# Kernel tuning notes

Measured on AMD Instinct MI355X. Metric: run time of the kernel, lower is better.

## Reference

```python
import jax, jax.numpy as jnp
import numpy as np

EMB = 768
HEADS = 12
HEAD_DIM = EMB // HEADS


def setup_inputs() -> dict:
    key = jax.random.key(0)
    k1, k2, k3, k4 = jax.random.split(key, 4)
    x = jax.random.normal(k1, (8, 1024, EMB), dtype=jnp.float32)
    # Dense kernels, TF default glorot-ish scale approximated with small normals
    w_qkv = jax.random.normal(k2, (EMB, 3 * EMB), dtype=jnp.float32) * 0.02
    w_out = jax.random.normal(k3, (EMB, EMB), dtype=jnp.float32) * 0.02
    b_out = jnp.zeros((EMB,), dtype=jnp.float32)
    return {"x": x, "w_qkv": w_qkv, "w_out": w_out, "b_out": b_out}


def reference(x, w_qkv, w_out, b_out):
    B, S, E = x.shape
    qkv = jnp.einsum("bse,ef->bsf", x, w_qkv)                 # [B,S,3E]
    qkv = qkv.reshape(B, S, 3, HEADS, HEAD_DIM)
    qkv = jnp.transpose(qkv, (2, 0, 3, 1, 4))                  # [3,B,H,S,D]
    q, k, v = qkv[0], qkv[1], qkv[2]
    scale = jnp.float32(HEAD_DIM) ** -0.5
    # Blocked loop in source computes exact full (non-causal) attention:
    # every query block attends to all keys -> equivalent to standard SDPA.
    scores = jnp.einsum("bhqd,bhkd->bhqk", q, k) * scale       # [B,H,S,S]
    probs = jax.nn.softmax(scores, axis=-1)
    out = jnp.einsum("bhqk,bhkd->bhqd", probs, v)              # [B,H,S,D]
    out = jnp.transpose(out, (0, 2, 1, 3)).reshape(B, S, E)
    return jnp.einsum("bse,ef->bsf", out, w_out) + b_out
```

## Files before the change

kernel.cpp:

```cpp
#include <hip/hip_runtime.h>

typedef float f32x4 __attribute__((ext_vector_type(4)));
typedef short bf16x8 __attribute__((ext_vector_type(8)));

#define MFMA_BF16(a, b, c) __builtin_amdgcn_mfma_f32_16x16x32_bf16((a), (b), (c), 0, 0, 0)

#define GLDS16(gp, lp) __builtin_amdgcn_global_load_lds( \
    (const __attribute__((address_space(1))) unsigned int*)(gp), \
    (__attribute__((address_space(3))) unsigned int*)(lp), 16, 0, 0)

__device__ __forceinline__ ushort f2bf(float f) {
    unsigned int u = __float_as_uint(f);
    return (ushort)((u + 0x7FFFu + ((u >> 16) & 1u)) >> 16);
}

__device__ __forceinline__ float fexp2(float x) {
#if __has_builtin(__builtin_amdgcn_exp2f)
    return __builtin_amdgcn_exp2f(x);
#else
    return exp2f(x);
#endif
}

__global__ __launch_bounds__(256) void prep_kernel(
    const float* __restrict__ x, const float* __restrict__ wq, const float* __restrict__ wo,
    ushort* __restrict__ xb, ushort* __restrict__ wqbt, ushort* __restrict__ wobt)
{
    __shared__ float tile[32][33];
    const int bid = blockIdx.x;
    if (bid < 2048) {
        const float4* src = (const float4*)x;
        ushort4* dst = (ushort4*)xb;
        for (int i = bid * 256 + threadIdx.x; i < 1572864; i += 2048 * 256) {
            float4 v = src[i];
            ushort4 o;
            o.x = f2bf(v.x); o.y = f2bf(v.y); o.z = f2bf(v.z); o.w = f2bf(v.w);
            dst[i] = o;
        }
        return;
    }
    const float* src; ushort* dst; int K, N, bx, by;
    if (bid < 3776) {
        const int L = bid - 2048;
        src = wq; dst = wqbt; K = 768; N = 2304; bx = L % 72; by = L / 72;
    } else {
        const int L = bid - 3776;
        src = wo; dst = wobt; K = 768; N = 768; bx = L % 24; by = L / 24;
    }
    const int n0 = bx * 32, k0 = by * 32;
    const int c = threadIdx.x & 31, rb = threadIdx.x >> 5;
    #pragma unroll
    for (int i = 0; i < 4; ++i)
        tile[i * 8 + rb][c] = src[(size_t)(k0 + i * 8 + rb) * N + n0 + c];
    __syncthreads();
    #pragma unroll
    for (int i = 0; i < 4; ++i) {
        int nr = i * 8 + rb;
        dst[(size_t)(n0 + nr) * K + k0 + c] = f2bf(tile[c][nr]);
    }
}

__global__ __launch_bounds__(512) void gemm_qkv_mfma(
    const ushort* __restrict__ A, const ushort* __restrict__ Bt,
    ushort* __restrict__ Qo, ushort* __restrict__ Ko, ushort* __restrict__ Vo)
{
    __shared__ ushort Al[3][16384];
    __shared__ ushort Bl[3][8192];
    const int tid = threadIdx.x, lane = tid & 63;
    const int wv = tid >> 6, lo = lane & 15, hi = lane >> 4;
    const int wr = wv >> 1, wc = wv & 1;
    const int L = blockIdx.x;
    const int nid = (L & 7) * 72 + (L >> 3);
    const int n0 = (nid % 18) * 128, m0 = (nid / 18) * 256;

    auto stageA = [&](int bi, int k0) {
        #pragma unroll
        for (int it = 0; it < 4; ++it) {
            const int p = it * 512 + tid;
            const int row = p >> 3, ch = (p & 7) ^ (row & 7);
            GLDS16(A + (size_t)(m0 + row) * 768 + k0 + ch * 8,
                   &Al[bi][(it * 512 + (tid & 448)) * 8]);
        }
    };
    auto stageB = [&](int bi, int k0) {
        #pragma unroll
        for (int it = 0; it < 2; ++it) {
            const int p = it * 512 + tid;
            const int row = p >> 3, ch = (p & 7) ^ (row & 7);
            GLDS16(Bt + (size_t)(n0 + row) * 768 + k0 + ch * 8,
                   &Bl[bi][(it * 512 + (tid & 448)) * 8]);
        }
    };

    f32x4 acc[4][4];
    #pragma unroll
    for (int i = 0; i < 4; ++i)
        #pragma unroll
        for (int j = 0; j < 4; ++j)
            acc[i][j] = (f32x4){0.f, 0.f, 0.f, 0.f};

    const int region = n0 / 768;
    const int h = ((n0 % 768) >> 6) + wc;

    stageA(0, 0);  stageB(0, 0);
    stageA(1, 64); stageB(1, 64);

    int cur = 0;
    for (int t = 0; t < 12; ++t) {
        if (t < 11) asm volatile("s_waitcnt vmcnt(6)" ::: "memory");
        else        asm volatile("s_waitcnt vmcnt(0)" ::: "memory");
        __builtin_amdgcn_s_barrier();
        asm volatile("" ::: "memory");
        if (t + 2 < 12) {
            const int nb = cur ? cur - 1 : 2;
            stageA(nb, (t + 2) * 64);
            stageB(nb, (t + 2) * 64);
        }
        #pragma unroll
        for (int ks = 0; ks < 2; ++ks) {
            bf16x8 af[4], bfr[4];
            #pragma unroll
            for (int i = 0; i < 4; ++i) {
                const int ra = wr * 64 + i * 16 + lo;
                af[i] = *(const bf16x8*)&Al[cur][ra * 64 + (((ks * 4 + hi) ^ (ra & 7)) * 8)];
                const int rb = wc * 64 + i * 16 + lo;
                bfr[i] = *(const bf16x8*)&Bl[cur][rb * 64 + (((ks * 4 + hi) ^ (rb & 7)) * 8)];
            }
            if (region == 2) {
                #pragma unroll
                for (int mi = 0; mi < 4; ++mi)
                    #pragma unroll
                    for (int nj = 0; nj < 4; ++nj)
                        acc[mi][nj] = MFMA_BF16(af[mi], bfr[nj], acc[mi][nj]);
            } else {
                #pragma unroll
                for (int mi = 0; mi < 4; ++mi)
                    #pragma unroll
                    for (int nj = 0; nj < 4; ++nj)
                        acc[mi][nj] = MFMA_BF16(bfr[nj], af[mi], acc[mi][nj]);
            }
        }
        cur = cur == 2 ? 0 : cur + 1;
    }

    if (region == 2) {
        #pragma unroll
        for (int mi = 0; mi < 4; ++mi) {
            const int m4 = m0 + wr * 64 + mi * 16 + hi * 4;
            const int b = m4 >> 10, s = m4 & 1023;
            #pragma unroll
            for (int nj = 0; nj < 4; ++nj) {
                const int d = nj * 16 + lo;
                ushort4 pk;
                pk.x = f2bf(acc[mi][nj][0]); pk.y = f2bf(acc[mi][nj][1]);
                pk.z = f2bf(acc[mi][nj][2]); pk.w = f2bf(acc[mi][nj][3]);
                *(ushort4*)&Vo[((size_t)(b * 12 + h) * 64 + d) * 1024 + s] = pk;
            }
        }
    } else {
        ushort* dst = region ? Ko : Qo;
        const float sc = region ? 1.0f : 0.18033688011112042f;
        #pragma unroll
        for (int mi = 0; mi < 4; ++mi) {
            const int s_idx = m0 + wr * 64 + mi * 16 + lo;
            const int b = s_idx >> 10, s = s_idx & 1023;
            const size_t base = ((size_t)(b * 12 + h) * 1024 + s) * 64;
            #pragma unroll
            for (int nj = 0; nj < 4; ++nj) {
                ushort4 pk;
                pk.x = f2bf(acc[mi][nj][0] * sc); pk.y = f2bf(acc[mi][nj][1] * sc);
                pk.z = f2bf(acc[mi][nj][2] * sc); pk.w = f2bf(acc[mi][nj][3] * sc);
                *(ushort4*)&dst[base + nj * 16 + hi * 4] = pk;
            }
        }
    }
}

__global__ __launch_bounds__(256) void attn_mfma_kernel(
    const ushort* __restrict__ Qg, const ushort* __restrict__ Kg,
    const ushort* __restrict__ Vg, ushort* __restrict__ AO)
{
    __shared__ ushort Kl[2][4096];
    __shared__ ushort Vl[2][4096];
    __shared__ ushort Pl[4][32 * 72];

    const int tid = threadIdx.x, lane = tid & 63;
    const int wv = tid >> 6, lo = lane & 15, hi = lane >> 4;
    const int L = blockIdx.x;
    const int xcd = L & 7, g = L >> 3;
    const int qb = g / 12;
    const int bh = xcd * 12 + (g % 12);
    const int b = bh / 12, h = bh % 12;
    const size_t kvbase = (size_t)bh * (1024 * 64);

    bf16x8 qa[2][2];
    const int qrow0 = qb * 128 + wv * 32;
    #pragma unroll
    for (int mi = 0; mi < 2; ++mi)
        #pragma unroll
        for (int ks = 0; ks < 2; ++ks)
            qa[mi][ks] = *(const bf16x8*)&Qg[kvbase + (size_t)(qrow0 + mi * 16 + lo) * 64 + ks * 32 + hi * 8];

    f32x4 o[2][4];
    float lp[2] = {0.f, 0.f};
    #pragma unroll
    for (int mi = 0; mi < 2; ++mi)
        #pragma unroll
        for (int dj = 0; dj < 4; ++dj) o[mi][dj] = (f32x4){0.f, 0.f, 0.f, 0.f};

    auto stage = [&](int bi, int kt) {
        #pragma unroll
        for (int it = 0; it < 2; ++it) {
            const int p = it * 256 + tid;
            const int row = p >> 3, ch = (p & 7) ^ (row & 7);
            GLDS16(Kg + kvbase + (size_t)(kt + row) * 64 + ch * 8, &Kl[bi][(it * 256 + (tid & 192)) * 8]);
        }
        #pragma unroll
        for (int it = 0; it < 2; ++it) {
            const int p = it * 256 + tid;
            const int row = p >> 3, ch = (p & 7) ^ (row & 7);
            GLDS16(Vg + kvbase + (size_t)row * 1024 + kt + ch * 8, &Vl[bi][(it * 256 + (tid & 192)) * 8]);
        }
    };

    stage(0, 0);
    __syncthreads();

    for (int t = 0; t < 16; ++t) {
        const int cur = t & 1;
        if (t < 15) stage(cur ^ 1, (t + 1) * 64);

        f32x4 s[2][4];
        #pragma unroll
        for (int mi = 0; mi < 2; ++mi)
            #pragma unroll
            for (int nj = 0; nj < 4; ++nj) s[mi][nj] = (f32x4){0.f, 0.f, 0.f, 0.f};
        #pragma unroll
        for (int ks = 0; ks < 2; ++ks) {
            bf16x8 kb[4];
            #pragma unroll
            for (int nj = 0; nj < 4; ++nj) {
                const int key = nj * 16 + lo, c = ks * 4 + hi;
                kb[nj] = *(const bf16x8*)&Kl[cur][key * 64 + ((c ^ (key & 7)) * 8)];
            }
            #pragma unroll
            for (int mi = 0; mi < 2; ++mi)
                #pragma unroll
                for (int nj = 0; nj < 4; ++nj)
                    s[mi][nj] = MFMA_BF16(kb[nj], qa[mi][ks], s[mi][nj]);
        }

        #pragma unroll
        for (int mi = 0; mi < 2; ++mi) {
            #pragma unroll
            for (int nj = 0; nj < 4; ++nj) {
                const unsigned int u0 = __float_as_uint(fexp2(s[mi][nj][0]));
                const unsigned int u1 = __float_as_uint(fexp2(s[mi][nj][1]));
                const unsigned int u2 = __float_as_uint(fexp2(s[mi][nj][2]));
                const unsigned int u3 = __float_as_uint(fexp2(s[mi][nj][3]));
                const float t0 = __uint_as_float(u0 & 0xFFFF0000u);
                const float t1 = __uint_as_float(u1 & 0xFFFF0000u);
                const float t2 = __uint_as_float(u2 & 0xFFFF0000u);
                const float t3 = __uint_as_float(u3 & 0xFFFF0000u);
                lp[mi] += (t0 + t1) + (t2 + t3);
                ushort4 pk;
                pk.x = (ushort)(u0 >> 16); pk.y = (ushort)(u1 >> 16);
                pk.z = (ushort)(u2 >> 16); pk.w = (ushort)(u3 >> 16);
                *(ushort4*)&Pl[wv][(mi * 16 + lo) * 72 + nj * 16 + hi * 4] = pk;
            }
        }

        #pragma unroll
        for (int ks = 0; ks < 2; ++ks) {
            bf16x8 pa[2];
            #pragma unroll
            for (int mi = 0; mi < 2; ++mi)
                pa[mi] = *(const bf16x8*)&Pl[wv][(mi * 16 + lo) * 72 + ks * 32 + hi * 8];
            bf16x8 vb[4];
            #pragma unroll
            for (int dj = 0; dj < 4; ++dj) {
                const int d = dj * 16 + lo, c = ks * 4 + hi;
                vb[dj] = *(const bf16x8*)&Vl[cur][d * 64 + ((c ^ (d & 7)) * 8)];
            }
            #pragma unroll
            for (int mi = 0; mi < 2; ++mi)
                #pragma unroll
                for (int dj = 0; dj < 4; ++dj)
                    o[mi][dj] = MFMA_BF16(pa[mi], vb[dj], o[mi][dj]);
        }
        __syncthreads();
    }

    #pragma unroll
    for (int mi = 0; mi < 2; ++mi) {
        float l = lp[mi];
        l += __shfl_xor(l, 16);
        l += __shfl_xor(l, 32);
        #pragma unroll
        for (int r = 0; r < 4; ++r) {
            const float lr = __shfl(l, hi * 4 + r, 16);
            const float rcp = 1.0f / lr;
            const int srow = qrow0 + mi * 16 + hi * 4 + r;
            #pragma unroll
            for (int dj = 0; dj < 4; ++dj)
                AO[((size_t)(b * 1024 + srow)) * 768 + h * 64 + dj * 16 + lo] =
                    f2bf(o[mi][dj][r] * rcp);
        }
    }
}

__global__ __launch_bounds__(256) void gemm_out_mfma(
    const ushort* __restrict__ A, const ushort* __restrict__ Bt,
    const float* __restrict__ bias, float* __restrict__ C)
{
    __shared__ ushort Al[2][4096];
    __shared__ ushort Bl[2][4096];
    const int tid = threadIdx.x, lane = tid & 63;
    const int wv = tid >> 6, lo = lane & 15, hi = lane >> 4;
    const int wr = wv >> 1, wc = wv & 1;
    const int L = blockIdx.x + 6 * blockIdx.y;
    const int nid = (L & 7) * 48 + (L >> 3);
    const int n0 = (nid % 6) * 128, m0 = (nid / 6) * 128;

    auto stage = [&](int bi, int k0) {
        #pragma unroll
        for (int it = 0; it < 2; ++it) {
            const int p = it * 256 + tid;
            const int row = p >> 2, ch = (p & 3) ^ ((row >> 1) & 3);
            GLDS16(A + (size_t)(m0 + row) * 768 + k0 + ch * 8, &Al[bi][(it * 256 + (tid & 192)) * 8]);
            GLDS16(Bt + (size_t)(n0 + row) * 768 + k0 + ch * 8, &Bl[bi][(it * 256 + (tid & 192)) * 8]);
        }
    };

    f32x4 acc[4][4];
    #pragma unroll
    for (int i = 0; i < 4; ++i)
        #pragma unroll
        for (int j = 0; j < 4; ++j)
            acc[i][j] = (f32x4){0.f, 0.f, 0.f, 0.f};

    stage(0, 0);
    __syncthreads();
    for (int kt = 0; kt < 24; ++kt) {
        const int cur = kt & 1;
        if (kt < 23) stage(cur ^ 1, (kt + 1) * 32);
        bf16x8 af[4], bfr[4];
        #pragma unroll
        for (int i = 0; i < 4; ++i) {
            const int ra = wr * 64 + i * 16 + lo;
            af[i] = *(const bf16x8*)&Al[cur][ra * 32 + ((hi ^ ((ra >> 1) & 3)) * 8)];
            const int rb = wc * 64 + i * 16 + lo;
            bfr[i] = *(const bf16x8*)&Bl[cur][rb * 32 + ((hi ^ ((rb >> 1) & 3)) * 8)];
        }
        #pragma unroll
        for (int mi = 0; mi < 4; ++mi)
            #pragma unroll
            for (int nj = 0; nj < 4; ++nj)
                acc[mi][nj] = MFMA_BF16(bfr[nj], af[mi], acc[mi][nj]);
        __syncthreads();
    }

    const int ncol0 = n0 + wc * 64;
    #pragma unroll
    for (int mi = 0; mi < 4; ++mi) {
        const int m = m0 + wr * 64 + mi * 16 + lo;
        #pragma unroll
        for (int nj = 0; nj < 4; ++nj) {
            const int nb = ncol0 + nj * 16 + hi * 4;
            const float4 bv = *reinterpret_cast<const float4*>(&bias[nb]);
            float4 ov;
            ov.x = acc[mi][nj][0] + bv.x; ov.y = acc[mi][nj][1] + bv.y;
            ov.z = acc[mi][nj][2] + bv.z; ov.w = acc[mi][nj][3] + bv.w;
            *reinterpret_cast<float4*>(&C[(size_t)m * 768 + nb]) = ov;
        }
    }
}

extern "C" void kernel_launch(void* const* d_in, const int* in_sizes, int n_in,
                              void* d_out, int out_size, void* d_ws, size_t ws_size,
                              hipStream_t stream) {
    const float* x     = (const float*)d_in[0];
    const float* w_qkv = (const float*)d_in[1];
    const float* w_out = (const float*)d_in[2];
    const float* b_out = (const float*)d_in[3];
    float* out = (float*)d_out;

    (void)in_sizes; (void)n_in; (void)out_size; (void)ws_size;

    ushort* xb   = (ushort*)d_ws;
    ushort* wqbt = xb + 6291456;
    ushort* wobt = wqbt + 1769472;
    ushort* Qs   = wobt + 589824;
    ushort* Ks   = Qs + 6291456;
    ushort* Vt   = Ks + 6291456;
    ushort* AO   = Vt + 6291456;

    prep_kernel<<<4352, 256, 0, stream>>>(x, w_qkv, w_out, xb, wqbt, wobt);
    gemm_qkv_mfma<<<576, 512, 0, stream>>>(xb, wqbt, Qs, Ks, Vt);
    attn_mfma_kernel<<<768, 256, 0, stream>>>(Qs, Ks, Vt, AO);
    gemm_out_mfma<<<dim3(6, 64), 256, 0, stream>>>(AO, wobt, b_out, out);
}
```

Before: 134.6 us.

## Retile QKV GEMM to 128x128 double-buffered blocks and unify out-projection pipeline

The QKV projection GEMM moves from 512-thread 256x128 tiles with a triple-buffered LDS ring to 256-thread 128x128 tiles with double buffering, doubling the grid to 1152 blocks. Each k-step now ends with an extra barrier before the next tile is staged. The output-projection GEMM adopts the same pipeline: K-step 64 instead of 32, an 8-chunk XOR swizzle, two tiles prefetched ahead, and a 1D grid. The aim is more blocks and waves per CU and fewer barrier iterations in the out GEMM, at the cost of less reuse of each tile and one extra barrier per step.

```diff
diff --git a/kernel.cpp b/kernel.cpp
--- a/kernel.cpp
+++ b/kernel.cpp
@@ -60,35 +60,33 @@
     }
 }
 
-__global__ __launch_bounds__(512) void gemm_qkv_mfma(
+__global__ __launch_bounds__(256) void gemm_qkv_mfma(
     const ushort* __restrict__ A, const ushort* __restrict__ Bt,
     ushort* __restrict__ Qo, ushort* __restrict__ Ko, ushort* __restrict__ Vo)
 {
-    __shared__ ushort Al[3][16384];
-    __shared__ ushort Bl[3][8192];
+    __shared__ ushort Al[2][8192];
+    __shared__ ushort Bl[2][8192];
     const int tid = threadIdx.x, lane = tid & 63;
     const int wv = tid >> 6, lo = lane & 15, hi = lane >> 4;
     const int wr = wv >> 1, wc = wv & 1;
     const int L = blockIdx.x;
-    const int nid = (L & 7) * 72 + (L >> 3);
-    const int n0 = (nid % 18) * 128, m0 = (nid / 18) * 256;
-
-    auto stageA = [&](int bi, int k0) {
+    const int nid = (L & 7) * 144 + (L >> 3);
+    const int n0 = (nid % 18) * 128, m0 = (nid / 18) * 128;
+
+    auto stage = [&](int bi, int k0) {
         #pragma unroll
         for (int it = 0; it < 4; ++it) {
-            const int p = it * 512 + tid;
+            const int p = it * 256 + tid;
             const int row = p >> 3, ch = (p & 7) ^ (row & 7);
             GLDS16(A + (size_t)(m0 + row) * 768 + k0 + ch * 8,
-                   &Al[bi][(it * 512 + (tid & 448)) * 8]);
-        }
-    };
-    auto stageB = [&](int bi, int k0) {
-        #pragma unroll
-        for (int it = 0; it < 2; ++it) {
-            const int p = it * 512 + tid;
+                   &Al[bi][(it * 256 + (tid & 192)) * 8]);
+        }
+        #pragma unroll
+        for (int it = 0; it < 4; ++it) {
+            const int p = it * 256 + tid;
             const int row = p >> 3, ch = (p & 7) ^ (row & 7);
             GLDS16(Bt + (size_t)(n0 + row) * 768 + k0 + ch * 8,
-                   &Bl[bi][(it * 512 + (tid & 448)) * 8]);
+                   &Bl[bi][(it * 256 + (tid & 192)) * 8]);
         }
     };
 
@@ -102,20 +100,16 @@
     const int region = n0 / 768;
     const int h = ((n0 % 768) >> 6) + wc;
 
-    stageA(0, 0);  stageB(0, 0);
-    stageA(1, 64); stageB(1, 64);
+    stage(0, 0);
+    stage(1, 64);
 
     int cur = 0;
     for (int t = 0; t < 12; ++t) {
-        if (t < 11) asm volatile("s_waitcnt vmcnt(6)" ::: "memory");
+        if (t < 11) asm volatile("s_waitcnt vmcnt(8)" ::: "memory");
         else        asm volatile("s_waitcnt vmcnt(0)" ::: "memory");
         __builtin_amdgcn_s_barrier();
         asm volatile("" ::: "memory");
-        if (t + 2 < 12) {
-            const int nb = cur ? cur - 1 : 2;
-            stageA(nb, (t + 2) * 64);
-            stageB(nb, (t + 2) * 64);
-        }
+
         #pragma unroll
         for (int ks = 0; ks < 2; ++ks) {
             bf16x8 af[4], bfr[4];
@@ -140,7 +134,12 @@
                         acc[mi][nj] = MFMA_BF16(bfr[nj], af[mi], acc[mi][nj]);
             }
         }
-        cur = cur == 2 ? 0 : cur + 1;
+
+        asm volatile("s_waitcnt lgkmcnt(0)" ::: "memory");
+        __builtin_amdgcn_s_barrier();
+        asm volatile("" ::: "memory");
+        if (t + 2 < 12) stage(cur, (t + 2) * 64);
+        cur ^= 1;
     }
 
     if (region == 2) {
@@ -313,22 +312,29 @@
     const ushort* __restrict__ A, const ushort* __restrict__ Bt,
     const float* __restrict__ bias, float* __restrict__ C)
 {
-    __shared__ ushort Al[2][4096];
-    __shared__ ushort Bl[2][4096];
+    __shared__ ushort Al[2][8192];
+    __shared__ ushort Bl[2][8192];
     const int tid = threadIdx.x, lane = tid & 63;
     const int wv = tid >> 6, lo = lane & 15, hi = lane >> 4;
     const int wr = wv >> 1, wc = wv & 1;
-    const int L = blockIdx.x + 6 * blockIdx.y;
+    const int L = blockIdx.x;
     const int nid = (L & 7) * 48 + (L >> 3);
     const int n0 = (nid % 6) * 128, m0 = (nid / 6) * 128;
 
     auto stage = [&](int bi, int k0) {
         #pragma unroll
-        for (int it = 0; it < 2; ++it) {
-            const int p = it * 256 + tid;
-            const int row = p >> 2, ch = (p & 3) ^ ((row >> 1) & 3);
-            GLDS16(A + (size_t)(m0 + row) * 768 + k0 + ch * 8, &Al[bi][(it * 256 + (tid & 192)) * 8]);
-            GLDS16(Bt + (size_t)(n0 + row) * 768 + k0 + ch * 8, &Bl[bi][(it * 256 + (tid & 192)) * 8]);
+        for (int it = 0; it < 4; ++it) {
+            const int p = it * 256 + tid;
+            const int row = p >> 3, ch = (p & 7) ^ (row & 7);
+            GLDS16(A + (size_t)(m0 + row) * 768 + k0 + ch * 8,
+                   &Al[bi][(it * 256 + (tid & 192)) * 8]);
+        }
+        #pragma unroll
+        for (int it = 0; it < 4; ++it) {
+            const int p = it * 256 + tid;
+            const int row = p >> 3, ch = (p & 7) ^ (row & 7);
+            GLDS16(Bt + (size_t)(n0 + row) * 768 + k0 + ch * 8,
+                   &Bl[bi][(it * 256 + (tid & 192)) * 8]);
         }
     };
 
@@ -340,24 +346,37 @@
             acc[i][j] = (f32x4){0.f, 0.f, 0.f, 0.f};
 
     stage(0, 0);
-    __syncthreads();
-    for (int kt = 0; kt < 24; ++kt) {
-        const int cur = kt & 1;
-        if (kt < 23) stage(cur ^ 1, (kt + 1) * 32);
-        bf16x8 af[4], bfr[4];
-        #pragma unroll
-        for (int i = 0; i < 4; ++i) {
-            const int ra = wr * 64 + i * 16 + lo;
-            af[i] = *(const bf16x8*)&Al[cur][ra * 32 + ((hi ^ ((ra >> 1) & 3)) * 8)];
-            const int rb = wc * 64 + i * 16 + lo;
-            bfr[i] = *(const bf16x8*)&Bl[cur][rb * 32 + ((hi ^ ((rb >> 1) & 3)) * 8)];
-        }
-        #pragma unroll
-        for (int mi = 0; mi < 4; ++mi)
-            #pragma unroll
-            for (int nj = 0; nj < 4; ++nj)
-                acc[mi][nj] = MFMA_BF16(bfr[nj], af[mi], acc[mi][nj]);
-        __syncthreads();
+    stage(1, 64);
+
+    int cur = 0;
+    for (int t = 0; t < 12; ++t) {
+        if (t < 11) asm volatile("s_waitcnt vmcnt(8)" ::: "memory");
+        else        asm volatile("s_waitcnt vmcnt(0)" ::: "memory");
+        __builtin_amdgcn_s_barrier();
+        asm volatile("" ::: "memory");
+
+        #pragma unroll
+        for (int ks = 0; ks < 2; ++ks) {
+            bf16x8 af[4], bfr[4];
+            #pragma unroll
+            for (int i = 0; i < 4; ++i) {
+                const int ra = wr * 64 + i * 16 + lo;
+                af[i] = *(const bf16x8*)&Al[cur][ra * 64 + (((ks * 4 + hi) ^ (ra & 7)) * 8)];
+                const int rb = wc * 64 + i * 16 + lo;
+                bfr[i] = *(const bf16x8*)&Bl[cur][rb * 64 + (((ks * 4 + hi) ^ (rb & 7)) * 8)];
+            }
+            #pragma unroll
+            for (int mi = 0; mi < 4; ++mi)
+                #pragma unroll
+                for (int nj = 0; nj < 4; ++nj)
+                    acc[mi][nj] = MFMA_BF16(bfr[nj], af[mi], acc[mi][nj]);
+        }
+
+        asm volatile("s_waitcnt lgkmcnt(0)" ::: "memory");
+        __builtin_amdgcn_s_barrier();
+        asm volatile("" ::: "memory");
+        if (t + 2 < 12) stage(cur, (t + 2) * 64);
+        cur ^= 1;
     }
 
     const int ncol0 = n0 + wc * 64;
@@ -396,7 +415,7 @@
     ushort* AO   = Vt + 6291456;
 
     prep_kernel<<<4352, 256, 0, stream>>>(x, w_qkv, w_out, xb, wqbt, wobt);
-    gemm_qkv_mfma<<<576, 512, 0, stream>>>(xb, wqbt, Qs, Ks, Vt);
+    gemm_qkv_mfma<<<1152, 256, 0, stream>>>(xb, wqbt, Qs, Ks, Vt);
     attn_mfma_kernel<<<768, 256, 0, stream>>>(Qs, Ks, Vt, AO);
-    gemm_out_mfma<<<dim3(6, 64), 256, 0, stream>>>(AO, wobt, b_out, out);
-}
+    gemm_out_mfma<<<384, 256, 0, stream>>>(AO, wobt, b_out, out);
+}
```

Result: faster. 122.9 us, median of 2 (-8.7%).
